# Kernel tuning notes

Measured on AMD Instinct MI355X. Metric: run time of the kernel, lower is better.

Reference implementation:

```python
import jax, jax.numpy as jnp
import numpy as np

N = 10000
NHID = 128
E = 320000

def setup_inputs() -> dict:
    key = jax.random.key(0)
    k1, k2, k3 = jax.random.split(key, 3)
    x = jax.random.normal(k1, (N, NHID), dtype=jnp.float32)
    edge_index = jax.random.randint(k2, (2, E), 0, N, dtype=jnp.int64)
    # GCNConv weight (glorot-ish scale) and bias
    W = jax.random.normal(k3, (NHID, NHID), dtype=jnp.float32) * (1.0 / np.sqrt(NHID))
    b = jnp.zeros((NHID,), dtype=jnp.float32)
    return {"x": x, "edge_index": edge_index, "W": W, "b": b}

def _gcn_conv(x, edge_index, W, b):
    n = x.shape[0]
    # linear transform first (PyG GCNConv order)
    xw = x @ W  # [N, nhid]
    # add self-loops with weight 1
    loop = jnp.arange(n, dtype=edge_index.dtype)
    row = jnp.concatenate([edge_index[0], loop])  # source
    col = jnp.concatenate([edge_index[1], loop])  # target
    ew = jnp.ones(row.shape[0], dtype=x.dtype)
    # symmetric normalization: deg from incoming edges at target
    deg = jax.ops.segment_sum(ew, col, num_segments=n)
    dinv = jnp.where(deg > 0, jax.lax.rsqrt(deg), 0.0)
    norm = dinv[row] * ew * dinv[col]  # [E+N]
    # message passing: aggregate norm * xw[src] at target
    msgs = norm[:, None] * xw[row]  # [E+N, nhid]
    out = jax.ops.segment_sum(msgs, col, num_segments=n)
    return out + b

def reference(x, edge_index, W, b):
    h = jax.nn.relu(_gcn_conv(x, edge_index, W, b))
    # dropout in eval mode -> identity
    return h @ h.T  # [N, N] reconstructed structure
```

## Files before the change

kernel.cpp:

```cpp
#include <hip/hip_runtime.h>
#include <hip/hip_bf16.h>

#define N_NODES 10000
#define NHID 128
#define NEDGE 320000

typedef float  float4_t  __attribute__((ext_vector_type(4)));
typedef float  float2_t  __attribute__((ext_vector_type(2)));
typedef short  short8    __attribute__((ext_vector_type(8)));

__global__ void k_detect(const int* __restrict__ ei32, int* __restrict__ flag) {
    __shared__ int s_or;
    if (threadIdx.x == 0) s_or = 0;
    __syncthreads();
    int v = ei32[2 * threadIdx.x + 1] | ei32[2 * ((int)threadIdx.x + 256) + 1];
    if (v) atomicOr(&s_or, 1);
    __syncthreads();
    if (threadIdx.x == 0) flag[0] = (s_or == 0) ? 1 : 0;
}

__device__ inline int edge_at(const int* __restrict__ ei, int mode, int idx) {
    return mode ? ei[2 * idx] : ei[idx];
}

__global__ void k_count(const int* __restrict__ ei, const int* __restrict__ flag,
                        int* __restrict__ cnt) {
    int e = blockIdx.x * 256 + threadIdx.x;
    if (e >= NEDGE) return;
    int mode = flag[0];
    int dst = edge_at(ei, mode, NEDGE + e);
    atomicAdd(&cnt[dst], 1);
}

#define SCAN_T 1024
#define SCAN_CH 10
__global__ __launch_bounds__(SCAN_T)
void k_scan(const int* __restrict__ cnt, int* __restrict__ off, int* __restrict__ cur) {
    __shared__ int sums[SCAN_T];
    int t = threadIdx.x;
    int base = t * SCAN_CH;
    int loc[SCAN_CH];
    int s = 0;
#pragma unroll
    for (int i = 0; i < SCAN_CH; i++) {
        int idx = base + i;
        int v = (idx < N_NODES) ? cnt[idx] : 0;
        loc[i] = s;
        s += v;
    }
    sums[t] = s;
    __syncthreads();
    for (int d = 1; d < SCAN_T; d <<= 1) {
        int v = (t >= d) ? sums[t - d] : 0;
        __syncthreads();
        sums[t] += v;
        __syncthreads();
    }
    int pre = (t == 0) ? 0 : sums[t - 1];
#pragma unroll
    for (int i = 0; i < SCAN_CH; i++) {
        int idx = base + i;
        if (idx < N_NODES) {
            int o = pre + loc[i];
            off[idx] = o;
            cur[idx] = o;
        }
    }
    if (t == SCAN_T - 1) off[N_NODES] = sums[t];
}

__global__ void k_dinv(const int* __restrict__ off, float* __restrict__ dinv) {
    int i = blockIdx.x * 256 + threadIdx.x;
    if (i < N_NODES) dinv[i] = rsqrtf((float)(off[i + 1] - off[i]) + 1.0f);
}

__global__ void k_fill(const int* __restrict__ ei, const int* __restrict__ flag,
                       int* __restrict__ cur, int* __restrict__ srcIdx) {
    int e = blockIdx.x * 256 + threadIdx.x;
    if (e >= NEDGE) return;
    int mode = flag[0];
    int src = edge_at(ei, mode, e);
    int dst = edge_at(ei, mode, NEDGE + e);
    int pos = atomicAdd(&cur[dst], 1);
    srcIdx[pos] = src;
}

__global__ void k_xw(const float* __restrict__ x, const float* __restrict__ W,
                     float* __restrict__ xw) {
    __shared__ float xs[8 * 128];
    int t = threadIdx.x;
    int rowBase = blockIdx.x * 8;
    {
        int idx = t * 4;
        int r = idx >> 7;
        int rr = rowBase + r;
        float4_t v = {0.f, 0.f, 0.f, 0.f};
        if (rr < N_NODES) v = *(const float4_t*)&x[rr * 128 + (idx & 127)];
        *(float4_t*)&xs[idx] = v;
    }
    __syncthreads();
    int c = t & 31;
    int rloc = t >> 5;
    int row = rowBase + rloc;
    float4_t acc = {0.f, 0.f, 0.f, 0.f};
#pragma unroll 8
    for (int k = 0; k < 128; k++) {
        float xv = xs[rloc * 128 + k];
        float4_t wv = *(const float4_t*)&W[k * 128 + c * 4];
        acc += xv * wv;
    }
    if (row < N_NODES) *(float4_t*)&xw[row * 128 + c * 4] = acc;
}

__global__ __launch_bounds__(256)
void k_gather_h(const int* __restrict__ srcIdx, const int* __restrict__ off,
                const float* __restrict__ xw, const float* __restrict__ dinv,
                const float* __restrict__ b, __hip_bfloat16* __restrict__ hbf) {
    int t = threadIdx.x;
    int lane = t & 63;
    int node = blockIdx.x * 4 + (t >> 6);
    if (node >= N_NODES) return;
    int f = lane * 2;
    float di = dinv[node];
    float2_t acc = di * *(const float2_t*)&xw[node * 128 + f];
    int e = off[node], end = off[node + 1];
    for (; e + 2 <= end; e += 2) {
        int s0 = srcIdx[e], s1 = srcIdx[e + 1];
        float w0 = dinv[s0], w1 = dinv[s1];
        float2_t v0 = *(const float2_t*)&xw[s0 * 128 + f];
        float2_t v1 = *(const float2_t*)&xw[s1 * 128 + f];
        acc += w0 * v0;
        acc += w1 * v1;
    }
    if (e < end) {
        int s0 = srcIdx[e];
        acc += dinv[s0] * *(const float2_t*)&xw[s0 * 128 + f];
    }
    float2_t bb = *(const float2_t*)&b[f];
    float2_t v = di * acc + bb;
    __hip_bfloat16* dst = &hbf[node * 128 + f];
    dst[0] = __float2bfloat16(fmaxf(v.x, 0.0f));
    dst[1] = __float2bfloat16(fmaxf(v.y, 0.0f));
}

#define LDSLD 136
__global__ __launch_bounds__(256, 2)
void k_gemm(const __hip_bfloat16* __restrict__ h, float* __restrict__ out) {
    __shared__ unsigned short As[128][LDSLD];
    __shared__ unsigned short Bs[128][LDSLD];
    int by = blockIdx.y, bx = blockIdx.x;
    int t = threadIdx.x;
    const unsigned short* hu = (const unsigned short*)h;

#pragma unroll
    for (int it = 0; it < 8; it++) {
        int c = t + it * 256;
        int row = c >> 4;
        int col8 = (c & 15) * 8;
        int gra = by * 128 + row;
        float4_t va = {0.f, 0.f, 0.f, 0.f};
        if (gra < N_NODES) va = *(const float4_t*)&hu[gra * 128 + col8];
        *(float4_t*)&As[row][col8] = va;
        int grb = bx * 128 + row;
        float4_t vb = {0.f, 0.f, 0.f, 0.f};
        if (grb < N_NODES) vb = *(const float4_t*)&hu[grb * 128 + col8];
        *(float4_t*)&Bs[row][col8] = vb;
    }
    __syncthreads();

    int lane = t & 63, w = t >> 6;
    int wm = (w >> 1) * 64, wn = (w & 1) * 64;
    int quad = lane >> 4, l16 = lane & 15;

    float4_t acc[4][4] = {};
    short8 a_frag[4], b_frag[4];

#pragma unroll
    for (int ks = 0; ks < 4; ks++) {
        int k0 = ks * 32 + quad * 8;
#pragma unroll
        for (int mi = 0; mi < 4; mi++)
            a_frag[mi] = *(const short8*)&As[wm + mi * 16 + l16][k0];
#pragma unroll
        for (int ni = 0; ni < 4; ni++)
            b_frag[ni] = *(const short8*)&Bs[wn + ni * 16 + l16][k0];
#pragma unroll
        for (int mi = 0; mi < 4; mi++)
#pragma unroll
            for (int ni = 0; ni < 4; ni++)
                acc[mi][ni] = __builtin_amdgcn_mfma_f32_16x16x32_bf16(
                    a_frag[mi], b_frag[ni], acc[mi][ni], 0, 0, 0);
    }

#pragma unroll
    for (int mi = 0; mi < 4; mi++) {
        int gr0 = by * 128 + wm + mi * 16 + quad * 4;
#pragma unroll
        for (int r = 0; r < 4; r++) {
            int grow = gr0 + r;
            if (grow >= N_NODES) continue;
            long rowoff = (long)grow * N_NODES;
#pragma unroll
            for (int ni = 0; ni < 4; ni++) {
                int gcol = bx * 128 + wn + ni * 16 + l16;
                if (gcol < N_NODES)
                    __builtin_nontemporal_store(acc[mi][ni][r], &out[rowoff + gcol]);
            }
        }
    }
}

extern "C" void kernel_launch(void* const* d_in, const int* in_sizes, int n_in,
                              void* d_out, int out_size, void* d_ws, size_t ws_size,
                              hipStream_t stream) {
    const float* x  = (const float*)d_in[0];
    const int*   ei = (const int*)d_in[1];
    const float* W  = (const float*)d_in[2];
    const float* b  = (const float*)d_in[3];
    float* out = (float*)d_out;

    char* ws = (char*)d_ws;
    float* xw   = (float*)(ws);
    float* dinv = (float*)(ws + 5120000);
    int*   flg  = (int*)  (ws + 5160192);
    int*   cnt  = (int*)  (ws + 5160448);
    int*   off  = (int*)  (ws + 5200640);
    int*   cur  = (int*)  (ws + 5240832);
    int*   srcI = (int*)  (ws + 5281024);
    __hip_bfloat16* hbf = (__hip_bfloat16*)(ws + 6561024);

    hipMemsetAsync(cnt, 0, (size_t)N_NODES * sizeof(int), stream);
    k_detect<<<1, 256, 0, stream>>>(ei, flg);
    k_count<<<(NEDGE + 255) / 256, 256, 0, stream>>>(ei, flg, cnt);
    k_scan<<<1, SCAN_T, 0, stream>>>(cnt, off, cur);
    k_dinv<<<(N_NODES + 255) / 256, 256, 0, stream>>>(off, dinv);
    k_xw<<<(N_NODES + 7) / 8, 256, 0, stream>>>(x, W, xw);
    k_fill<<<(NEDGE + 255) / 256, 256, 0, stream>>>(ei, flg, cur, srcI);
    k_gather_h<<<(N_NODES + 3) / 4, 256, 0, stream>>>(srcI, off, xw, dinv, b, hbf);
    dim3 g((N_NODES + 127) / 128, (N_NODES + 127) / 128);
    k_gemm<<<g, 256, 0, stream>>>(hbf, out);
}
```

Measured before the change: 552.8 us.

## Use 32x32 MFMA with XOR-swizzled LDS in gemm, fuse dinv into scan

The output GEMM switches from 16x16x32 to 32x32x16 bf16 MFMA tiles and replaces the padded LDS layout with an XOR swizzle to avoid bank conflicts. The store pattern changes to match the 32x32 accumulator layout, so each lane writes 32 consecutive columns per row group. The separate dinv kernel is folded into the scan kernel to save a launch. Risk: the new store pattern may coalesce differently on the write-bound 400MB output.

```diff
diff --git a/kernel.cpp b/kernel.cpp
--- a/kernel.cpp
+++ b/kernel.cpp
@@ -5,9 +5,10 @@
 #define NHID 128
 #define NEDGE 320000
 
-typedef float  float4_t  __attribute__((ext_vector_type(4)));
-typedef float  float2_t  __attribute__((ext_vector_type(2)));
-typedef short  short8    __attribute__((ext_vector_type(8)));
+typedef float  float4_t   __attribute__((ext_vector_type(4)));
+typedef float  float2_t   __attribute__((ext_vector_type(2)));
+typedef float  float16_t  __attribute__((ext_vector_type(16)));
+typedef short  short8     __attribute__((ext_vector_type(8)));
 
 __global__ void k_detect(const int* __restrict__ ei32, int* __restrict__ flag) {
     __shared__ int s_or;
@@ -35,7 +36,8 @@
 #define SCAN_T 1024
 #define SCAN_CH 10
 __global__ __launch_bounds__(SCAN_T)
-void k_scan(const int* __restrict__ cnt, int* __restrict__ off, int* __restrict__ cur) {
+void k_scan(const int* __restrict__ cnt, int* __restrict__ off, int* __restrict__ cur,
+            float* __restrict__ dinv) {
     __shared__ int sums[SCAN_T];
     int t = threadIdx.x;
     int base = t * SCAN_CH;
@@ -64,14 +66,10 @@
             int o = pre + loc[i];
             off[idx] = o;
             cur[idx] = o;
+            dinv[idx] = rsqrtf((float)cnt[idx] + 1.0f);
         }
     }
     if (t == SCAN_T - 1) off[N_NODES] = sums[t];
-}
-
-__global__ void k_dinv(const int* __restrict__ off, float* __restrict__ dinv) {
-    int i = blockIdx.x * 256 + threadIdx.x;
-    if (i < N_NODES) dinv[i] = rsqrtf((float)(off[i + 1] - off[i]) + 1.0f);
 }
 
 __global__ void k_fill(const int* __restrict__ ei, const int* __restrict__ flag,
@@ -143,11 +141,10 @@
     dst[1] = __float2bfloat16(fmaxf(v.y, 0.0f));
 }
 
-#define LDSLD 136
 __global__ __launch_bounds__(256, 2)
 void k_gemm(const __hip_bfloat16* __restrict__ h, float* __restrict__ out) {
-    __shared__ unsigned short As[128][LDSLD];
-    __shared__ unsigned short Bs[128][LDSLD];
+    __shared__ unsigned short As[128][128];
+    __shared__ unsigned short Bs[128][128];
     int by = blockIdx.y, bx = blockIdx.x;
     int t = threadIdx.x;
     const unsigned short* hu = (const unsigned short*)h;
@@ -156,58 +153,62 @@
     for (int it = 0; it < 8; it++) {
         int c = t + it * 256;
         int row = c >> 4;
-        int col8 = (c & 15) * 8;
+        int ch  = c & 15;
+        int sl  = ch ^ (row & 15);
         int gra = by * 128 + row;
         float4_t va = {0.f, 0.f, 0.f, 0.f};
-        if (gra < N_NODES) va = *(const float4_t*)&hu[gra * 128 + col8];
-        *(float4_t*)&As[row][col8] = va;
+        if (gra < N_NODES) va = *(const float4_t*)&hu[gra * 128 + ch * 8];
+        *(float4_t*)&As[row][sl * 8] = va;
         int grb = bx * 128 + row;
         float4_t vb = {0.f, 0.f, 0.f, 0.f};
-        if (grb < N_NODES) vb = *(const float4_t*)&hu[grb * 128 + col8];
-        *(float4_t*)&Bs[row][col8] = vb;
+        if (grb < N_NODES) vb = *(const float4_t*)&hu[grb * 128 + ch * 8];
+        *(float4_t*)&Bs[row][sl * 8] = vb;
     }
     __syncthreads();
 
     int lane = t & 63, w = t >> 6;
     int wm = (w >> 1) * 64, wn = (w & 1) * 64;
-    int quad = lane >> 4, l16 = lane & 15;
-
-    float4_t acc[4][4] = {};
-    short8 a_frag[4], b_frag[4];
-
-#pragma unroll
-    for (int ks = 0; ks < 4; ks++) {
-        int k0 = ks * 32 + quad * 8;
-#pragma unroll
-        for (int mi = 0; mi < 4; mi++)
-            a_frag[mi] = *(const short8*)&As[wm + mi * 16 + l16][k0];
-#pragma unroll
-        for (int ni = 0; ni < 4; ni++)
-            b_frag[ni] = *(const short8*)&Bs[wn + ni * 16 + l16][k0];
-#pragma unroll
-        for (int mi = 0; mi < 4; mi++)
-#pragma unroll
-            for (int ni = 0; ni < 4; ni++)
-                acc[mi][ni] = __builtin_amdgcn_mfma_f32_16x16x32_bf16(
-                    a_frag[mi], b_frag[ni], acc[mi][ni], 0, 0, 0);
-    }
-
-#pragma unroll
-    for (int mi = 0; mi < 4; mi++) {
-        int gr0 = by * 128 + wm + mi * 16 + quad * 4;
-#pragma unroll
-        for (int r = 0; r < 4; r++) {
-            int grow = gr0 + r;
-            if (grow >= N_NODES) continue;
-            long rowoff = (long)grow * N_NODES;
-#pragma unroll
-            for (int ni = 0; ni < 4; ni++) {
-                int gcol = bx * 128 + wn + ni * 16 + l16;
-                if (gcol < N_NODES)
-                    __builtin_nontemporal_store(acc[mi][ni][r], &out[rowoff + gcol]);
+    int l32 = lane & 31;
+    int hi  = lane >> 5;
+
+    float16_t acc[2][2] = {};
+    short8 af[2], bf[2];
+
+#pragma unroll
+    for (int ks = 0; ks < 8; ks++) {
+        int ch = ks * 2 + hi;
+#pragma unroll
+        for (int mi = 0; mi < 2; mi++) {
+            int r = wm + mi * 32 + l32;
+            af[mi] = *(const short8*)&As[r][(ch ^ (r & 15)) * 8];
+        }
+#pragma unroll
+        for (int ni = 0; ni < 2; ni++) {
+            int r = wn + ni * 32 + l32;
+            bf[ni] = *(const short8*)&Bs[r][(ch ^ (r & 15)) * 8];
+        }
+#pragma unroll
+        for (int mi = 0; mi < 2; mi++)
+#pragma unroll
+            for (int ni = 0; ni < 2; ni++)
+                acc[mi][ni] = __builtin_amdgcn_mfma_f32_32x32x16_bf16(
+                    af[mi], bf[ni], acc[mi][ni], 0, 0, 0);
+    }
+
+#pragma unroll
+    for (int mi = 0; mi < 2; mi++)
+#pragma unroll
+        for (int ni = 0; ni < 2; ni++) {
+            int gc = bx * 128 + wn + ni * 32 + l32;
+            if (gc >= N_NODES) continue;
+#pragma unroll
+            for (int reg = 0; reg < 16; reg++) {
+                int gr = by * 128 + wm + mi * 32 + (reg & 3) + 8 * (reg >> 2) + 4 * hi;
+                if (gr < N_NODES)
+                    __builtin_nontemporal_store(acc[mi][ni][reg],
+                                                &out[(long)gr * N_NODES + gc]);
             }
         }
-    }
 }
 
 extern "C" void kernel_launch(void* const* d_in, const int* in_sizes, int n_in,
@@ -232,8 +233,7 @@
     hipMemsetAsync(cnt, 0, (size_t)N_NODES * sizeof(int), stream);
     k_detect<<<1, 256, 0, stream>>>(ei, flg);
     k_count<<<(NEDGE + 255) / 256, 256, 0, stream>>>(ei, flg, cnt);
-    k_scan<<<1, SCAN_T, 0, stream>>>(cnt, off, cur);
-    k_dinv<<<(N_NODES + 255) / 256, 256, 0, stream>>>(off, dinv);
+    k_scan<<<1, SCAN_T, 0, stream>>>(cnt, off, cur, dinv);
     k_xw<<<(N_NODES + 7) / 8, 256, 0, stream>>>(x, W, xw);
     k_fill<<<(NEDGE + 255) / 256, 256, 0, stream>>>(ei, flg, cur, srcI);
     k_gather_h<<<(N_NODES + 3) / 4, 256, 0, stream>>>(srcI, off, xw, dinv, b, hbf);
```

Result: faster. 534.3 us (-3.4%).
